# Kernel tuning notes

Hardware: AMD Instinct MI355X
Metric: run time of the kernel (lower is better)

The kernel has to match this reference:

```python
import jax, jax.numpy as jnp
import numpy as np

N = 100000        # nodes
E = 3200000       # edges (avg in-degree ~32)
NG = 64           # graphs in batch
F_IN = 64         # num_node_features
AVG_LOG = float(np.log(33.0))   # avg log-degree baked from deg (avg degree 32)
BN_EPS = 1e-5
STD_EPS = 1e-5

def _glorot(key, fi, fo):
    lim = float(np.sqrt(6.0 / (fi + fo)))
    return jax.random.uniform(key, (fi, fo), jnp.float32, -lim, lim)

def setup_inputs():
    key = jax.random.key(0)
    ks = jax.random.split(key, 16)
    inp = {
        'x': jax.random.normal(ks[0], (N, F_IN), jnp.float32),
        'edge_index': jax.random.randint(ks[1], (2, E), 0, N),
        'batch': jnp.sort(jax.random.randint(ks[2], (N,), 0, NG)),
    }
    dims = [(F_IN, 96), (96, 64), (64, 32), (32, 20)]
    for i, (fi, fo) in enumerate(dims):
        inp[f'w{i}'] = _glorot(ks[3 + i], 13 * fi, fo)  # (4 aggr * 3 scalers + 1 self) * F_in
        inp[f'b{i}'] = jnp.zeros((fo,), jnp.float32)
    for i, c in enumerate([96, 64, 20]):
        inp[f'g{i}'] = jnp.ones((c,), jnp.float32)
        inp[f'be{i}'] = jnp.zeros((c,), jnp.float32)
    inp['w_lin'] = _glorot(ks[10], 20, 11)
    inp['b_lin'] = jnp.zeros((11,), jnp.float32)
    return inp

def _pna_layer(x, src, dst, cnt, degc, W, b):
    m = x[src]                                          # [E, F] gather of neighbor feats
    inv = (1.0 / degc)[:, None]
    mean = jax.ops.segment_sum(m, dst, N) * inv
    mean_sq = jax.ops.segment_sum(m * m, dst, N) * inv
    std = jnp.sqrt(jax.nn.relu(mean_sq - mean * mean) + STD_EPS)
    has = (cnt > 0)[:, None]
    mn = jnp.where(has, jax.ops.segment_min(m, dst, N), 0.0)
    mx = jnp.where(has, jax.ops.segment_max(m, dst, N), 0.0)
    agg = jnp.concatenate([mean, mn, mx, std], axis=-1)  # [N, 4F]
    logd = jnp.log(degc + 1.0)[:, None]
    out = jnp.concatenate([agg, agg * (logd / AVG_LOG), agg * (AVG_LOG / logd)], axis=-1)  # [N, 12F]
    out = jnp.concatenate([x, out], axis=-1)             # [N, 13F] self + scaled aggregations
    return out @ W + b

def _bn(x, g, b):
    mu = x.mean(0)
    var = x.var(0)  # biased var: matches torch BatchNorm training forward
    return (x - mu) * jax.lax.rsqrt(var + BN_EPS) * g + b

def _forward(x, edge_index, batch, w0, b0, w1, b1, w2, b2, w3, b3,
             g0, be0, g1, be1, g2, be2, w_lin, b_lin):
    src, dst = edge_index[0], edge_index[1]
    cnt = jax.ops.segment_sum(jnp.ones((E,), x.dtype), dst, N)  # in-degree
    degc = jnp.maximum(cnt, 1.0)
    h = jax.nn.relu(_bn(_pna_layer(x, src, dst, cnt, degc, w0, b0), g0, be0))
    h = jax.nn.relu(_bn(_pna_layer(h, src, dst, cnt, degc, w1, b1), g1, be1))
    h = jax.nn.relu(_pna_layer(h, src, dst, cnt, degc, w2, b2))
    h = _bn(_pna_layer(h, src, dst, cnt, degc, w3, b3), g2, be2)
    gcnt = jnp.maximum(jax.ops.segment_sum(jnp.ones((N,), h.dtype), batch, NG), 1.0)
    z = jax.ops.segment_sum(h, batch, NG) / gcnt[:, None]       # global mean pool [NG, 20]
    out = jax.nn.softmax(z @ w_lin + b_lin, axis=-1)            # dropout identity (eval)
    return out, z

def reference(x, edge_index, batch, w0, b0, w1, b1, w2, b2, w3, b3,
              g0, be0, g1, be1, g2, be2, w_lin, b_lin):
    return _forward(x, edge_index, batch, w0, b0, w1, b1, w2, b2, w3, b3,
                    g0, be0, g1, be1, g2, be2, w_lin, b_lin)
```

## Files before the change

### kernel.cpp

```cpp
#include <hip/hip_runtime.h>

#define NN 100000
#define NGRAPH 64
#define NPART 8
#define NPB 12500
#define DB 16
#define PW_C 2048
#define AVGLOG 3.4965075614664802f

using f32x2 = __attribute__((ext_vector_type(2))) float;
using f32x4 = __attribute__((ext_vector_type(4))) float;
using f16x2 = __attribute__((ext_vector_type(2))) _Float16;
using f16x8 = __attribute__((ext_vector_type(8))) _Float16;
using f16x4 = __attribute__((ext_vector_type(4))) _Float16;
using i32x4 = __attribute__((ext_vector_type(4))) int;

__global__ __launch_bounds__(256) void k_pcnt(const int* __restrict__ ei,
                                              int* __restrict__ pcnt, int E, int W) {
  const int w = blockIdx.x * 4 + (threadIdx.x >> 6);
  const int lane = threadIdx.x & 63;
  if (w >= W) return;
  int c[NPART];
#pragma unroll
  for (int b = 0; b < NPART; ++b) c[b] = 0;
  const long long base = (long long)w * PW_C;
  for (int r = 0; r < PW_C / 256; ++r) {
    long long e0 = base + r * 256 + lane * 4;
    int bk[4] = {-1, -1, -1, -1};
    if (e0 + 3 < E) {
      i32x4 d = __builtin_nontemporal_load((const i32x4*)(ei + E + e0));
#pragma unroll
      for (int k = 0; k < 4; ++k) bk[k] = d[k] / NPB;
    } else {
#pragma unroll
      for (int k = 0; k < 4; ++k)
        if (e0 + k < E) bk[k] = ei[E + e0 + k] / NPB;
    }
#pragma unroll
    for (int b = 0; b < NPART; ++b) {
      int t = 0;
#pragma unroll
      for (int k = 0; k < 4; ++k) t += __popcll(__ballot(bk[k] == b));
      c[b] += t;
    }
  }
  if (lane == 0) {
#pragma unroll
    for (int b = 0; b < NPART; ++b) pcnt[w * NPART + b] = c[b];
  }
}

__global__ void k_pscan(const int* __restrict__ pcnt, int* __restrict__ pbase,
                        int* __restrict__ bcur, int W) {
  __shared__ int s[256];
  __shared__ int btot[NPART];
  const int t = threadIdx.x;
  const int per = (W + 255) / 256;
  for (int b = 0; b < NPART; ++b) {
    int loc = 0;
    const int w0 = t * per;
    for (int i = 0; i < per; ++i) {
      int w = w0 + i;
      if (w < W) loc += pcnt[w * NPART + b];
    }
    s[t] = loc;
    __syncthreads();
    for (int off = 1; off < 256; off <<= 1) {
      int u = (t >= off) ? s[t - off] : 0;
      __syncthreads();
      s[t] += u;
      __syncthreads();
    }
    int run = s[t] - loc;
    if (t == 255) btot[b] = s[255];
    for (int i = 0; i < per; ++i) {
      int w = w0 + i;
      if (w < W) {
        pbase[w * NPART + b] = run;
        run += pcnt[w * NPART + b];
      }
    }
    __syncthreads();
  }
  if (t < NPART) bcur[t] = btot[t];
}

__global__ __launch_bounds__(256) void k_pbin(const int* __restrict__ ei,
                                              const int* __restrict__ pbase,
                                              unsigned long long* __restrict__ bkt,
                                              int cap, int E, int W) {
  const int w = blockIdx.x * 4 + (threadIdx.x >> 6);
  const int lane = threadIdx.x & 63;
  if (w >= W) return;
  int off[NPART];
#pragma unroll
  for (int b = 0; b < NPART; ++b) off[b] = pbase[w * NPART + b];
  const unsigned long long lmask = (1ull << lane) - 1ull;
  const long long base = (long long)w * PW_C;
  for (int r = 0; r < PW_C / 256; ++r) {
    long long e0 = base + r * 256 + lane * 4;
    int bk[4] = {-1, -1, -1, -1};
    int sv[4], dv[4];
    if (e0 + 3 < E) {
      i32x4 d = __builtin_nontemporal_load((const i32x4*)(ei + E + e0));
      i32x4 s4 = __builtin_nontemporal_load((const i32x4*)(ei + e0));
#pragma unroll
      for (int k = 0; k < 4; ++k) { dv[k] = d[k]; sv[k] = s4[k]; bk[k] = d[k] / NPB; }
    } else {
#pragma unroll
      for (int k = 0; k < 4; ++k)
        if (e0 + k < E) { dv[k] = ei[E + e0 + k]; sv[k] = ei[e0 + k]; bk[k] = dv[k] / NPB; }
    }
#pragma unroll
    for (int k = 0; k < 4; ++k) {
#pragma unroll
      for (int b = 0; b < NPART; ++b) {
        unsigned long long m = __ballot(bk[k] == b);
        if (bk[k] == b) {
          int idx = off[b] + __popcll(m & lmask);
          bkt[(size_t)b * cap + idx] =
              ((unsigned long long)(unsigned)dv[k] << 32) | (unsigned)sv[k];
        }
        off[b] += __popcll(m);
      }
    }
  }
}

__global__ __launch_bounds__(256) void k_dhist(
    const unsigned long long* __restrict__ bkt, const int* __restrict__ bcur,
    int cap, int* __restrict__ dhist) {
  __shared__ int hist[NPB];
  const int p = blockIdx.x & (NPART - 1);
  const int b = blockIdx.x >> 3;
  const int tid = threadIdx.x;
  for (int i = tid; i < NPB; i += 256) hist[i] = 0;
  __syncthreads();
  const int n = bcur[p];
  const int chunk = (n + DB - 1) / DB;
  const int lo = b * chunk, hi = min(n, lo + chunk);
  const unsigned long long* base = bkt + (size_t)p * cap;
  const int plo = p * NPB;
  for (int i = lo + tid; i < hi; i += 256) {
    unsigned long long v = base[i];
    atomicAdd(&hist[(int)(v >> 32) - plo], 1);
  }
  __syncthreads();
  int* dst = dhist + ((size_t)p * DB + b) * NPB;
  for (int i = tid; i < NPB; i += 256) dst[i] = hist[i];
}

__global__ void k_mergesum(int* __restrict__ dhist, int* __restrict__ cnt,
                           int* __restrict__ bsum, int n) {
  __shared__ int s[256];
  int i = blockIdx.x * 256 + threadIdx.x;
  int acc = 0;
  if (i < n) {
    int p = i / NPB, li = i - p * NPB;
    int* hb = dhist + (size_t)p * DB * NPB + li;
#pragma unroll
    for (int b = 0; b < DB; ++b) {
      int t = hb[b * NPB];
      hb[b * NPB] = acc;
      acc += t;
    }
    cnt[i] = acc;
  }
  s[threadIdx.x] = acc;
  __syncthreads();
  for (int off = 128; off > 0; off >>= 1) {
    if (threadIdx.x < off) s[threadIdx.x] += s[threadIdx.x + off];
    __syncthreads();
  }
  if (threadIdx.x == 0) bsum[blockIdx.x] = s[0];
}

__global__ __launch_bounds__(256) void k_binfill(
    const unsigned long long* __restrict__ bkt, const int* __restrict__ bcur,
    int cap, const int* __restrict__ dhist, const int* __restrict__ row_ptr,
    int* __restrict__ colv) {
  __shared__ int rank[NPB];
  const int p = blockIdx.x & (NPART - 1);
  const int b = blockIdx.x >> 3;
  const int tid = threadIdx.x;
  const int plo = p * NPB;
  const int* soff = dhist + ((size_t)p * DB + b) * NPB;
  for (int li = tid; li < NPB; li += 256) rank[li] = row_ptr[plo + li] + soff[li];
  __syncthreads();
  const int n = bcur[p];
  const int chunk = (n + DB - 1) / DB;
  const int lo = b * chunk, hi = min(n, lo + chunk);
  const unsigned long long* base = bkt + (size_t)p * cap;
  for (int i = lo + tid; i < hi; i += 256) {
    unsigned long long v = base[i];
    int d = (int)(v >> 32);
    int s = (int)(v & 0xffffffffu);
    int pos = atomicAdd(&rank[d - plo], 1);
    colv[pos] = s;
  }
}

__global__ void k_scanb(const int* __restrict__ bsum, int* __restrict__ boff, int nb) {
  __shared__ int s[512];
  int t = threadIdx.x;
  int v = (t < nb) ? bsum[t] : 0;
  s[t] = v;
  __syncthreads();
  for (int off = 1; off < 512; off <<= 1) {
    int u = (t >= off) ? s[t - off] : 0;
    __syncthreads();
    s[t] += u;
    __syncthreads();
  }
  if (t < nb) boff[t] = s[t] - v;
}

__global__ void k_scatter(const int* __restrict__ cnt, const int* __restrict__ boff,
                          int* __restrict__ row_ptr, int n, int etot) {
  __shared__ int s[256];
  int i = blockIdx.x * 256 + threadIdx.x;
  int v = (i < n) ? cnt[i] : 0;
  s[threadIdx.x] = v;
  __syncthreads();
  for (int off = 1; off < 256; off <<= 1) {
    int u = (threadIdx.x >= off) ? s[threadIdx.x - off] : 0;
    __syncthreads();
    s[threadIdx.x] += u;
    __syncthreads();
  }
  if (i < n) row_ptr[i] = boff[blockIdx.x] + s[threadIdx.x] - v;
  if (i == 0) row_ptr[n] = etot;
}

__global__ void k_nodesc(const int* __restrict__ cnt, float* __restrict__ invd,
                         float* __restrict__ s1v, float* __restrict__ s2v, int n) {
  int i = blockIdx.x * 256 + threadIdx.x;
  if (i >= n) return;
  float degc = fmaxf((float)cnt[i], 1.f);
  invd[i] = 1.f / degc;
  float ld = logf(degc + 1.f);
  s1v[i] = ld * (1.f / AVGLOG);
  s2v[i] = AVGLOG / ld;
}

__global__ void k_wtprep(const float* __restrict__ W, _Float16* __restrict__ Wt,
                         int K, int FO, int FOP) {
  int i = blockIdx.x * 256 + threadIdx.x;
  if (i >= FOP * K) return;
  int nn = i / K, k = i - nn * K;
  float v = (nn < FO) ? W[k * FO + nn] : 0.f;
  int NT = FOP >> 4;
  int kt = k >> 5, q = (k >> 3) & 3, j = k & 7;
  int nt = nn >> 4, m = nn & 15;
  size_t idx = (((size_t)kt * NT + nt) * 64 + (q * 16 + m)) * 8 + j;
  Wt[idx] = (_Float16)v;
}

__global__ void k_xconv(const float* __restrict__ x, _Float16* __restrict__ x16, int n) {
  int i = blockIdx.x * 256 + threadIdx.x;
  if (i < n) x16[i] = (_Float16)x[i];
}

#define MFMA16(a, b, c) __builtin_amdgcn_mfma_f32_16x16x32_f16(a, b, c, 0, 0, 0)

template <int F, int FO, int FOP, bool RELU, bool STATS, typename OT>
__launch_bounds__(256, 2)
__global__ void k_fused(const _Float16* __restrict__ hin,
                        const int* __restrict__ row_ptr, const int* __restrict__ colv,
                        const float* __restrict__ invd,
                        const float* __restrict__ s1g, const float* __restrict__ s2g,
                        const _Float16* __restrict__ Wt, const float* __restrict__ bias,
                        OT* __restrict__ hout, float* __restrict__ csum,
                        float* __restrict__ csq) {
  constexpr int F32 = F / 32;
  constexpr int KTA = F / 8;
  constexpr int NT = FOP / 16;
  constexpr int PPW = (2 * NT) / 4;
  constexpr int XW = F + 8;
  constexpr int SEG = F / 8;
  constexpr int NP = SEG / 2;
  __shared__ __align__(16) _Float16 s_x[32][XW];
  __shared__ __align__(16) _Float16 s_a[2 * KTA * 512];
  __shared__ float s_cs[2][FOP];

  const int tid = threadIdx.x;
  const int n0 = blockIdx.x * 32;

  for (int idx = tid; idx < 32 * (F / 8); idx += 256) {
    int rr = idx / (F / 8), cc = idx % (F / 8);
    *(f16x8*)&s_x[rr][8 * cc] = *(const f16x8*)&hin[(size_t)(n0 + rr) * F + 8 * cc];
  }
  if (STATS)
    for (int u = tid; u < 2 * FOP; u += 256) (&s_cs[0][0])[u] = 0.f;

  {
    const int r = tid >> 3, g = tid & 7;
    const int n = n0 + r;
    const int e0 = row_ptr[n], e1 = row_ptr[n + 1];
    f32x2 sm[NP], sq[NP];
    f16x2 mn[NP], mx[NP];
    const _Float16 HPI = __builtin_bit_cast(_Float16, (unsigned short)0x7C00);
    const _Float16 HNI = __builtin_bit_cast(_Float16, (unsigned short)0xFC00);
#pragma unroll
    for (int p = 0; p < NP; ++p) {
      sm[p] = (f32x2){0.f, 0.f};
      sq[p] = (f32x2){0.f, 0.f};
      mn[p] = (f16x2){HPI, HPI};
      mx[p] = (f16x2){HNI, HNI};
    }

    auto loadrow = [&](const _Float16* ra, f16x2* pr) {
      if constexpr (SEG % 8 == 0) {
#pragma unroll
        for (int c = 0; c < SEG / 8; ++c) {
          f16x8 v = ((const f16x8*)ra)[c];
          pr[4 * c + 0] = (f16x2){v[0], v[1]};
          pr[4 * c + 1] = (f16x2){v[2], v[3]};
          pr[4 * c + 2] = (f16x2){v[4], v[5]};
          pr[4 * c + 3] = (f16x2){v[6], v[7]};
        }
      } else {
#pragma unroll
        for (int c = 0; c < SEG / 4; ++c) {
          f16x4 v = ((const f16x4*)ra)[c];
          pr[2 * c + 0] = (f16x2){v[0], v[1]};
          pr[2 * c + 1] = (f16x2){v[2], v[3]};
        }
      }
    };
    auto accum = [&](const f16x2* pr) {
#pragma unroll
      for (int p = 0; p < NP; ++p) {
        f32x2 f = __builtin_convertvector(pr[p], f32x2);
        sm[p] += f;
        sq[p] += f * f;
        mn[p] = __builtin_elementwise_min(mn[p], pr[p]);
        mx[p] = __builtin_elementwise_max(mx[p], pr[p]);
      }
    };

    int e = e0;
    for (; e + 1 < e1; e += 2) {
      int c0 = __builtin_nontemporal_load(&colv[e]);
      int c1 = __builtin_nontemporal_load(&colv[e + 1]);
      f16x2 r0[NP], r1[NP];
      loadrow(hin + (size_t)c0 * F + g * SEG, r0);
      loadrow(hin + (size_t)c1 * F + g * SEG, r1);
      accum(r0);
      accum(r1);
    }
    if (e < e1) {
      int c0 = __builtin_nontemporal_load(&colv[e]);
      f16x2 r0[NP];
      loadrow(hin + (size_t)c0 * F + g * SEG, r0);
      accum(r0);
    }

    float iv = invd[n];
    bool has = (e1 > e0);
    const int m = r & 15;
    const int mt = r >> 4;
#pragma unroll
    for (int c = 0; c < SEG / 4; ++c) {
      f16x4 vals[4];
#pragma unroll
      for (int l = 0; l < 4; ++l) {
        int j = 4 * c + l;
        int p = j >> 1, k = j & 1;
        float mean = sm[p][k] * iv;
        float var = sq[p][k] * iv - mean * mean;
        float sd = sqrtf(fmaxf(var, 0.f) + 1e-5f);
        vals[0][l] = (_Float16)mean;
        vals[1][l] = has ? mn[p][k] : (_Float16)0.f;
        vals[2][l] = has ? mx[p][k] : (_Float16)0.f;
        vals[3][l] = (_Float16)sd;
      }
      int f0 = g * SEG + 4 * c;
#pragma unroll
      for (int a = 0; a < 4; ++a) {
        int kk0 = a * F + f0;
        int kt = kk0 >> 5, q = (kk0 >> 3) & 3, j0 = kk0 & 7;
        *(f16x4*)&s_a[((size_t)(mt * KTA + kt)) * 512 + (q * 16 + m) * 8 + j0] = vals[a];
      }
    }
  }
  __syncthreads();

  const int w = tid >> 6, ln = tid & 63;
  const int lm = ln & 15, q = ln >> 4;
  const int mt = w & 1;
  const int arow = mt * 16 + lm;
  f32x4 acc0[PPW], acc1[PPW], acc2[PPW];
#pragma unroll
  for (int i = 0; i < PPW; ++i)
#pragma unroll
    for (int t = 0; t < 4; ++t) { acc0[i][t] = 0.f; acc1[i][t] = 0.f; acc2[i][t] = 0.f; }

#pragma unroll
  for (int kt = 0; kt < F32; ++kt) {
    f16x8 a = *(const f16x8*)&s_x[arow][kt * 32 + 8 * q];
#pragma unroll
    for (int i = 0; i < PPW; ++i) {
      int nt = (w >> 1) + 2 * i;
      f16x8 b = *(const f16x8*)&Wt[(((size_t)kt * NT + nt) * 64 + ln) * 8];
      acc0[i] = MFMA16(a, b, acc0[i]);
    }
  }
#pragma unroll
  for (int kt = 0; kt < KTA; ++kt) {
    f16x8 a = *(const f16x8*)&s_a[((size_t)(mt * KTA + kt)) * 512 + ln * 8];
#pragma unroll
    for (int i = 0; i < PPW; ++i) {
      int nt = (w >> 1) + 2 * i;
      f16x8 b0 = *(const f16x8*)&Wt[(((size_t)(F32 + kt) * NT + nt) * 64 + ln) * 8];
      acc0[i] = MFMA16(a, b0, acc0[i]);
      f16x8 b1 = *(const f16x8*)&Wt[(((size_t)(F32 + KTA + kt) * NT + nt) * 64 + ln) * 8];
      acc1[i] = MFMA16(a, b1, acc1[i]);
      f16x8 b2 = *(const f16x8*)&Wt[(((size_t)(F32 + 2 * KTA + kt) * NT + nt) * 64 + ln) * 8];
      acc2[i] = MFMA16(a, b2, acc2[i]);
    }
  }

  float s1r[4], s2r[4];
#pragma unroll
  for (int t = 0; t < 4; ++t) {
    int node = n0 + mt * 16 + q * 4 + t;
    s1r[t] = s1g[node];
    s2r[t] = s2g[node];
  }
#pragma unroll
  for (int i = 0; i < PPW; ++i) {
    int nt = (w >> 1) + 2 * i;
    int ncol = nt * 16 + lm;
    if (FOP == FO || ncol < FO) {
      float bs = bias[ncol];
      float cs = 0.f, cq = 0.f;
#pragma unroll
      for (int t = 0; t < 4; ++t) {
        int node = n0 + mt * 16 + q * 4 + t;
        float v = acc0[i][t] + s1r[t] * acc1[i][t] + s2r[t] * acc2[i][t] + bs;
        if (RELU) v = fmaxf(v, 0.f);
        hout[(size_t)node * FO + ncol] = (OT)v;
        cs += v;
        cq += v * v;
      }
      if (STATS) {
        atomicAdd(&s_cs[0][ncol], cs);
        atomicAdd(&s_cs[1][ncol], cq);
      }
    }
  }
  if (STATS) {
    __syncthreads();
    if (tid < FO) {
      atomicAdd(&csum[tid], s_cs[0][tid]);
      atomicAdd(&csq[tid], s_cs[1][tid]);
    }
  }
}

__global__ void k_bn16(_Float16* __restrict__ h, const float* __restrict__ csum,
                       const float* __restrict__ csq, const float* __restrict__ gg,
                       const float* __restrict__ be, int n, int fo, int relu) {
  int i = blockIdx.x * 256 + threadIdx.x;
  int total = (n * fo) >> 3;
  if (i >= total) return;
  int c0 = (i << 3) % fo;
  float invn = 1.f / (float)n;
  f16x8 v = *(const f16x8*)&h[(size_t)i << 3];
  f16x8 o;
#pragma unroll
  for (int j = 0; j < 8; ++j) {
    int c = c0 + j;
    float mu = csum[c] * invn;
    float var = csq[c] * invn - mu * mu;
    float rs = rsqrtf(var + 1e-5f);
    float x = ((float)v[j] - mu) * rs * gg[c] + be[c];
    if (relu) x = fmaxf(x, 0.f);
    o[j] = (_Float16)x;
  }
  *(f16x8*)&h[(size_t)i << 3] = o;
}

__global__ void k_bnf(float* __restrict__ h, const float* __restrict__ csum,
                      const float* __restrict__ csq, const float* __restrict__ gg,
                      const float* __restrict__ be, int n, int fo, int relu) {
  int i = blockIdx.x * 256 + threadIdx.x;
  if (i >= n * fo) return;
  int c = i % fo;
  float invn = 1.f / (float)n;
  float mu = csum[c] * invn;
  float var = csq[c] * invn - mu * mu;
  float rs = rsqrtf(var + 1e-5f);
  float v = (h[i] - mu) * rs * gg[c] + be[c];
  if (relu) v = fmaxf(v, 0.f);
  h[i] = v;
}

__global__ void k_pool(const float* __restrict__ h, const int* __restrict__ batch,
                       float* __restrict__ zsum, float* __restrict__ gcnt, int n) {
  __shared__ float sv[NGRAPH * 20];
  __shared__ float sc[NGRAPH];
  int tid = threadIdx.x;
  for (int u = tid; u < NGRAPH * 20; u += 256) sv[u] = 0.f;
  if (tid < NGRAPH) sc[tid] = 0.f;
  __syncthreads();
  int i = blockIdx.x * 256 + tid;
  if (i < n) {
    int g = batch[i];
    atomicAdd(&sc[g], 1.f);
    for (int j = 0; j < 20; ++j) atomicAdd(&sv[g * 20 + j], h[(size_t)i * 20 + j]);
  }
  __syncthreads();
  if (tid < NGRAPH && sc[tid] != 0.f) {
    atomicAdd(&gcnt[tid], sc[tid]);
    for (int j = 0; j < 20; ++j) atomicAdd(&zsum[tid * 20 + j], sv[tid * 20 + j]);
  }
}

__global__ void k_head(const float* __restrict__ zsum, const float* __restrict__ gcnt,
                       const float* __restrict__ wl, const float* __restrict__ bl,
                       float* __restrict__ out) {
  int g = threadIdx.x;
  if (g >= NGRAPH) return;
  float z[20];
  float icg = 1.f / fmaxf(gcnt[g], 1.f);
#pragma unroll
  for (int j = 0; j < 20; ++j) {
    z[j] = zsum[g * 20 + j] * icg;
    out[NGRAPH * 11 + g * 20 + j] = z[j];
  }
  float lo[11];
#pragma unroll
  for (int o = 0; o < 11; ++o) {
    float a = bl[o];
    for (int j = 0; j < 20; ++j) a += z[j] * wl[j * 11 + o];
    lo[o] = a;
  }
  float m = lo[0];
  for (int o = 1; o < 11; ++o) m = fmaxf(m, lo[o]);
  float s = 0.f;
  for (int o = 0; o < 11; ++o) { lo[o] = expf(lo[o] - m); s += lo[o]; }
  float is = 1.f / s;
  for (int o = 0; o < 11; ++o) out[g * 11 + o] = lo[o] * is;
}

static inline char* carve(char*& p, size_t bytes) {
  char* r = p;
  p += (bytes + 255) & ~(size_t)255;
  return r;
}

extern "C" void kernel_launch(void* const* d_in, const int* in_sizes, int n_in,
                              void* d_out, int out_size, void* d_ws, size_t ws_size,
                              hipStream_t stream) {
  const float* x = (const float*)d_in[0];
  const int* ei = (const int*)d_in[1];
  const int* batch = (const int*)d_in[2];
  const float* W0 = (const float*)d_in[3];
  const float* b0 = (const float*)d_in[4];
  const float* W1 = (const float*)d_in[5];
  const float* b1 = (const float*)d_in[6];
  const float* W2 = (const float*)d_in[7];
  const float* b2 = (const float*)d_in[8];
  const float* W3 = (const float*)d_in[9];
  const float* b3 = (const float*)d_in[10];
  const float* g0 = (const float*)d_in[11];
  const float* be0 = (const float*)d_in[12];
  const float* g1 = (const float*)d_in[13];
  const float* be1 = (const float*)d_in[14];
  const float* g2 = (const float*)d_in[15];
  const float* be2 = (const float*)d_in[16];
  const float* wl = (const float*)d_in[17];
  const float* bl = (const float*)d_in[18];
  float* out = (float*)d_out;

  const int E = in_sizes[1] / 2;
  const int NB = (NN + 255) / 256;
  const int BCAP = E / NPART + 65536;
  const int W = (E + PW_C - 1) / PW_C;
  const int GB = (W + 3) / 4;

  char* p = (char*)d_ws;
  int* cnt = (int*)carve(p, (size_t)NN * 4);
  int* row_ptr = (int*)carve(p, (size_t)(NN + 1) * 4);
  int* bsum = (int*)carve(p, 2048);
  int* boff = (int*)carve(p, 2048);
  int* bcur = (int*)carve(p, 256);
  int* pcnt = (int*)carve(p, (size_t)W * NPART * 4);
  int* pbase = (int*)carve(p, (size_t)W * NPART * 4);
  int* colv = (int*)carve(p, (size_t)E * 4);
  unsigned long long* bkt = (unsigned long long*)carve(p, (size_t)NPART * BCAP * 8);
  int* dhist = (int*)carve(p, (size_t)NPART * DB * NPB * 4);
  float* invd = (float*)carve(p, (size_t)NN * 4);
  float* s1v = (float*)carve(p, (size_t)NN * 4);
  float* s2v = (float*)carve(p, (size_t)NN * 4);
  _Float16* Wt0 = (_Float16*)carve(p, (size_t)96 * 832 * 2);
  _Float16* Wt1 = (_Float16*)carve(p, (size_t)64 * 1248 * 2);
  _Float16* Wt2 = (_Float16*)carve(p, (size_t)32 * 832 * 2);
  _Float16* Wt3 = (_Float16*)carve(p, (size_t)32 * 416 * 2);
  float* cs = (float*)carve(p, 192 * 4);
  float* csum = cs;
  float* csq = cs + 96;
  float* pacc = (float*)carve(p, (NGRAPH * 20 + NGRAPH) * 4);
  float* zsum = pacc;
  float* gcnt = pacc + NGRAPH * 20;
  _Float16* x16 = (_Float16*)carve(p, (size_t)NN * 64 * 2);
  _Float16* hA16 = (_Float16*)carve(p, (size_t)NN * 96 * 2);
  _Float16* hB16 = (_Float16*)carve(p, (size_t)NN * 96 * 2);
  float* h3 = (float*)x16;

  hipMemsetAsync(pacc, 0, (NGRAPH * 20 + NGRAPH) * 4, stream);
  k_pcnt<<<GB, 256, 0, stream>>>(ei, pcnt, E, W);
  k_pscan<<<1, 256, 0, stream>>>(pcnt, pbase, bcur, W);
  k_pbin<<<GB, 256, 0, stream>>>(ei, pbase, bkt, BCAP, E, W);
  k_dhist<<<NPART * DB, 256, 0, stream>>>(bkt, bcur, BCAP, dhist);
  k_mergesum<<<NB, 256, 0, stream>>>(dhist, cnt, bsum, NN);
  k_scanb<<<1, 512, 0, stream>>>(bsum, boff, NB);
  k_scatter<<<NB, 256, 0, stream>>>(cnt, boff, row_ptr, NN, E);
  k_nodesc<<<NB, 256, 0, stream>>>(cnt, invd, s1v, s2v, NN);
  k_binfill<<<NPART * DB, 256, 0, stream>>>(bkt, bcur, BCAP, dhist, row_ptr, colv);

  k_wtprep<<<(96 * 832 + 255) / 256, 256, 0, stream>>>(W0, Wt0, 832, 96, 96);
  k_wtprep<<<(64 * 1248 + 255) / 256, 256, 0, stream>>>(W1, Wt1, 1248, 64, 64);
  k_wtprep<<<(32 * 832 + 255) / 256, 256, 0, stream>>>(W2, Wt2, 832, 32, 32);
  k_wtprep<<<(32 * 416 + 255) / 256, 256, 0, stream>>>(W3, Wt3, 416, 20, 32);
  k_xconv<<<(NN * 64 + 255) / 256, 256, 0, stream>>>(x, x16, NN * 64);

  const int GP = NN / 32;

  hipMemsetAsync(cs, 0, 192 * 4, stream);
  k_fused<64, 96, 96, false, true, _Float16><<<GP, 256, 0, stream>>>(
      x16, row_ptr, colv, invd, s1v, s2v, Wt0, b0, hA16, csum, csq);
  k_bn16<<<(NN * 96 / 8 + 255) / 256, 256, 0, stream>>>(hA16, csum, csq, g0, be0, NN, 96, 1);

  hipMemsetAsync(cs, 0, 192 * 4, stream);
  k_fused<96, 64, 64, false, true, _Float16><<<GP, 256, 0, stream>>>(
      hA16, row_ptr, colv, invd, s1v, s2v, Wt1, b1, hB16, csum, csq);
  k_bn16<<<(NN * 64 / 8 + 255) / 256, 256, 0, stream>>>(hB16, csum, csq, g1, be1, NN, 64, 1);

  k_fused<64, 32, 32, true, false, _Float16><<<GP, 256, 0, stream>>>(
      hB16, row_ptr, colv, invd, s1v, s2v, Wt2, b2, hA16, csum, csq);

  hipMemsetAsync(cs, 0, 192 * 4, stream);
  k_fused<32, 20, 32, false, true, float><<<GP, 256, 0, stream>>>(
      hA16, row_ptr, colv, invd, s1v, s2v, Wt3, b3, h3, csum, csq);
  k_bnf<<<(NN * 20 + 255) / 256, 256, 0, stream>>>(h3, csum, csq, g2, be2, NN, 20, 0);

  k_pool<<<NB, 256, 0, stream>>>(h3, batch, zsum, gcnt, NN);
  k_head<<<1, 64, 0, stream>>>(zsum, gcnt, wl, bl, out);
}
```

Measured before the change: 866.3 us.

## Sub-bucket edges by source range within each destination partition for gather locality

Edge binning now uses 32 buckets (8 destination partitions × 4 source ranges), so within each destination partition the edges are grouped by source-node range. The CSR column order, and with it the neighbor gathers in the fused layers, should gain locality in the source features. The prefix scan is also parallelised across buckets, one block per bucket, with a small kernel that computes the bucket bases. In exchange the count and bin kernels do four times as many ballots per element, and one extra launch is added.

Result: no change. 853.1 us (-1.5%).

```diff
diff --git a/kernel.cpp b/kernel.cpp
--- a/kernel.cpp
+++ b/kernel.cpp
@@ -3,6 +3,9 @@
 #define NN 100000
 #define NGRAPH 64
 #define NPART 8
+#define SRCP 4
+#define SRCW 25000
+#define NBKT 32
 #define NPB 12500
 #define DB 16
 #define PW_C 2048
@@ -20,24 +23,25 @@
   const int w = blockIdx.x * 4 + (threadIdx.x >> 6);
   const int lane = threadIdx.x & 63;
   if (w >= W) return;
-  int c[NPART];
-#pragma unroll
-  for (int b = 0; b < NPART; ++b) c[b] = 0;
+  int c[NBKT];
+#pragma unroll
+  for (int b = 0; b < NBKT; ++b) c[b] = 0;
   const long long base = (long long)w * PW_C;
   for (int r = 0; r < PW_C / 256; ++r) {
     long long e0 = base + r * 256 + lane * 4;
     int bk[4] = {-1, -1, -1, -1};
     if (e0 + 3 < E) {
       i32x4 d = __builtin_nontemporal_load((const i32x4*)(ei + E + e0));
-#pragma unroll
-      for (int k = 0; k < 4; ++k) bk[k] = d[k] / NPB;
+      i32x4 s4 = __builtin_nontemporal_load((const i32x4*)(ei + e0));
+#pragma unroll
+      for (int k = 0; k < 4; ++k) bk[k] = (d[k] / NPB) * SRCP + s4[k] / SRCW;
     } else {
 #pragma unroll
       for (int k = 0; k < 4; ++k)
-        if (e0 + k < E) bk[k] = ei[E + e0 + k] / NPB;
-    }
-#pragma unroll
-    for (int b = 0; b < NPART; ++b) {
+        if (e0 + k < E) bk[k] = (ei[E + e0 + k] / NPB) * SRCP + ei[e0 + k] / SRCW;
+    }
+#pragma unroll
+    for (int b = 0; b < NBKT; ++b) {
       int t = 0;
 #pragma unroll
       for (int k = 0; k < 4; ++k) t += __popcll(__ballot(bk[k] == b));
@@ -46,55 +50,66 @@
   }
   if (lane == 0) {
 #pragma unroll
-    for (int b = 0; b < NPART; ++b) pcnt[w * NPART + b] = c[b];
+    for (int b = 0; b < NBKT; ++b) pcnt[w * NBKT + b] = c[b];
   }
 }
 
 __global__ void k_pscan(const int* __restrict__ pcnt, int* __restrict__ pbase,
-                        int* __restrict__ bcur, int W) {
+                        int* __restrict__ bt, int W) {
   __shared__ int s[256];
-  __shared__ int btot[NPART];
+  const int b = blockIdx.x;
   const int t = threadIdx.x;
   const int per = (W + 255) / 256;
-  for (int b = 0; b < NPART; ++b) {
-    int loc = 0;
-    const int w0 = t * per;
-    for (int i = 0; i < per; ++i) {
-      int w = w0 + i;
-      if (w < W) loc += pcnt[w * NPART + b];
-    }
-    s[t] = loc;
-    __syncthreads();
-    for (int off = 1; off < 256; off <<= 1) {
-      int u = (t >= off) ? s[t - off] : 0;
-      __syncthreads();
-      s[t] += u;
-      __syncthreads();
-    }
-    int run = s[t] - loc;
-    if (t == 255) btot[b] = s[255];
-    for (int i = 0; i < per; ++i) {
-      int w = w0 + i;
-      if (w < W) {
-        pbase[w * NPART + b] = run;
-        run += pcnt[w * NPART + b];
-      }
-    }
-    __syncthreads();
-  }
-  if (t < NPART) bcur[t] = btot[t];
+  int loc = 0;
+  const int w0 = t * per;
+  for (int i = 0; i < per; ++i) {
+    int w = w0 + i;
+    if (w < W) loc += pcnt[w * NBKT + b];
+  }
+  s[t] = loc;
+  __syncthreads();
+  for (int off = 1; off < 256; off <<= 1) {
+    int u = (t >= off) ? s[t - off] : 0;
+    __syncthreads();
+    s[t] += u;
+    __syncthreads();
+  }
+  int run = s[t] - loc;
+  if (t == 255) bt[b] = s[255];
+  for (int i = 0; i < per; ++i) {
+    int w = w0 + i;
+    if (w < W) {
+      pbase[w * NBKT + b] = run;
+      run += pcnt[w * NBKT + b];
+    }
+  }
+}
+
+__global__ void k_sbase(const int* __restrict__ bt, int* __restrict__ bbase,
+                        int* __restrict__ bcur, int cap) {
+  if (threadIdx.x == 0) {
+    for (int p = 0; p < NPART; ++p) {
+      int run = 0;
+      for (int sb = 0; sb < SRCP; ++sb) {
+        bbase[p * SRCP + sb] = p * cap + run;
+        run += bt[p * SRCP + sb];
+      }
+      bcur[p] = run;
+    }
+  }
 }
 
 __global__ __launch_bounds__(256) void k_pbin(const int* __restrict__ ei,
                                               const int* __restrict__ pbase,
+                                              const int* __restrict__ bbase,
                                               unsigned long long* __restrict__ bkt,
-                                              int cap, int E, int W) {
+                                              int E, int W) {
   const int w = blockIdx.x * 4 + (threadIdx.x >> 6);
   const int lane = threadIdx.x & 63;
   if (w >= W) return;
-  int off[NPART];
-#pragma unroll
-  for (int b = 0; b < NPART; ++b) off[b] = pbase[w * NPART + b];
+  int off[NBKT];
+#pragma unroll
+  for (int b = 0; b < NBKT; ++b) off[b] = bbase[b] + pbase[w * NBKT + b];
   const unsigned long long lmask = (1ull << lane) - 1ull;
   const long long base = (long long)w * PW_C;
   for (int r = 0; r < PW_C / 256; ++r) {
@@ -105,21 +120,28 @@
       i32x4 d = __builtin_nontemporal_load((const i32x4*)(ei + E + e0));
       i32x4 s4 = __builtin_nontemporal_load((const i32x4*)(ei + e0));
 #pragma unroll
-      for (int k = 0; k < 4; ++k) { dv[k] = d[k]; sv[k] = s4[k]; bk[k] = d[k] / NPB; }
+      for (int k = 0; k < 4; ++k) {
+        dv[k] = d[k];
+        sv[k] = s4[k];
+        bk[k] = (d[k] / NPB) * SRCP + s4[k] / SRCW;
+      }
     } else {
 #pragma unroll
       for (int k = 0; k < 4; ++k)
-        if (e0 + k < E) { dv[k] = ei[E + e0 + k]; sv[k] = ei[e0 + k]; bk[k] = dv[k] / NPB; }
+        if (e0 + k < E) {
+          dv[k] = ei[E + e0 + k];
+          sv[k] = ei[e0 + k];
+          bk[k] = (dv[k] / NPB) * SRCP + sv[k] / SRCW;
+        }
     }
 #pragma unroll
     for (int k = 0; k < 4; ++k) {
 #pragma unroll
-      for (int b = 0; b < NPART; ++b) {
+      for (int b = 0; b < NBKT; ++b) {
         unsigned long long m = __ballot(bk[k] == b);
         if (bk[k] == b) {
           int idx = off[b] + __popcll(m & lmask);
-          bkt[(size_t)b * cap + idx] =
-              ((unsigned long long)(unsigned)dv[k] << 32) | (unsigned)sv[k];
+          bkt[idx] = ((unsigned long long)(unsigned)dv[k] << 32) | (unsigned)sv[k];
         }
         off[b] += __popcll(m);
       }
@@ -587,8 +609,10 @@
   int* bsum = (int*)carve(p, 2048);
   int* boff = (int*)carve(p, 2048);
   int* bcur = (int*)carve(p, 256);
-  int* pcnt = (int*)carve(p, (size_t)W * NPART * 4);
-  int* pbase = (int*)carve(p, (size_t)W * NPART * 4);
+  int* bt = (int*)carve(p, 256);
+  int* bbase = (int*)carve(p, 256);
+  int* pcnt = (int*)carve(p, (size_t)W * NBKT * 4);
+  int* pbase = (int*)carve(p, (size_t)W * NBKT * 4);
   int* colv = (int*)carve(p, (size_t)E * 4);
   unsigned long long* bkt = (unsigned long long*)carve(p, (size_t)NPART * BCAP * 8);
   int* dhist = (int*)carve(p, (size_t)NPART * DB * NPB * 4);
@@ -612,8 +636,9 @@
 
   hipMemsetAsync(pacc, 0, (NGRAPH * 20 + NGRAPH) * 4, stream);
   k_pcnt<<<GB, 256, 0, stream>>>(ei, pcnt, E, W);
-  k_pscan<<<1, 256, 0, stream>>>(pcnt, pbase, bcur, W);
-  k_pbin<<<GB, 256, 0, stream>>>(ei, pbase, bkt, BCAP, E, W);
+  k_pscan<<<NBKT, 256, 0, stream>>>(pcnt, pbase, bt, W);
+  k_sbase<<<1, 64, 0, stream>>>(bt, bbase, bcur, BCAP);
+  k_pbin<<<GB, 256, 0, stream>>>(ei, pbase, bbase, bkt, E, W);
   k_dhist<<<NPART * DB, 256, 0, stream>>>(bkt, bcur, BCAP, dhist);
   k_mergesum<<<NB, 256, 0, stream>>>(dhist, cnt, bsum, NN);
   k_scanb<<<1, 512, 0, stream>>>(bsum, boff, NB);
```
